# Optimization experiments

Measured on AMD Instinct MI355X. Metric: run time of the kernel, lower is better.

The kernel has to match this reference:

```python
import jax, jax.numpy as jnp
import numpy as np

# Quantization constants from the original module
X_SCALE, X_ZP = 0.0215, -25
Y_SCALE, Y_ZP = 0.0176, 18


def setup_inputs() -> dict:
    key = jax.random.key(0)
    kx, ky = jax.random.split(key)
    K, N = 8192, 16384
    # int8 stand-ins (enum lacks int8); values fit int8 range
    x = jax.random.randint(kx, (K,), 0, 127, dtype=jnp.int32)
    y = jax.random.randint(ky, (K, N), 0, 127, dtype=jnp.int32)
    return {"x": x, "y": y}


def reference(x, y):
    # dequantize_per_tensor: (q - zero_point) * scale, in fp32
    xf = (x.astype(jnp.float32) - X_ZP) * X_SCALE   # [K]
    yf = (y.astype(jnp.float32) - Y_ZP) * Y_SCALE   # [K, N]
    # vector-matrix matmul -> [N]
    return xf @ yf
```

## Files before the change

### kernel.cpp

```cpp
#include <hip/hip_runtime.h>


constexpr int K = 8192;
constexpr int N = 16384;
constexpr float X_SCALE = 0.0215f;
constexpr int   X_ZP    = -25;
constexpr float Y_SCALE = 0.0176f;
constexpr int   Y_ZP    = 18;

constexpr int BLOCK = 256;
constexpr int VEC   = 4;
constexpr int COLS_PER_BLOCK = BLOCK * VEC;
constexpr int NBLK_N = N / COLS_PER_BLOCK;
constexpr int SPLIT_K = 128;
constexpr int KCHUNK = K / SPLIT_K;
constexpr int N4 = N / 4;

typedef int ivec4 __attribute__((ext_vector_type(4)));

__global__ __launch_bounds__(BLOCK, 8) void qgemv_partial(const int* __restrict__ x,
                                                          const ivec4* __restrict__ y,
                                                          ivec4* __restrict__ ws) {
    __shared__ int xs[KCHUNK];

    const int nb = blockIdx.x % NBLK_N;
    const int kc = blockIdx.x / NBLK_N;
    const int k0 = kc * KCHUNK;

    if (threadIdx.x < KCHUNK)
        xs[threadIdx.x] = x[k0 + threadIdx.x] - X_ZP;
    __syncthreads();

    const int col4 = nb * (COLS_PER_BLOCK / 4) + threadIdx.x;
    const ivec4* yv = y + (size_t)k0 * N4 + col4;

    int acc0 = 0, acc1 = 0, acc2 = 0, acc3 = 0;
    int sx = 0;

#pragma unroll 8
    for (int k = 0; k < KCHUNK; ++k) {
        ivec4 v = __builtin_nontemporal_load(&yv[(size_t)k * N4]);
        int a = xs[k];
        sx   += a;
        acc0 += a * v.x;
        acc1 += a * v.y;
        acc2 += a * v.z;
        acc3 += a * v.w;
    }

    const int corr = Y_ZP * sx;
    ivec4 p;
    p.x = acc0 - corr;
    p.y = acc1 - corr;
    p.z = acc2 - corr;
    p.w = acc3 - corr;
    ws[(size_t)kc * N4 + col4] = p;
}

__global__ __launch_bounds__(BLOCK) void qgemv_reduce(const ivec4* __restrict__ ws,
                                                      float* __restrict__ out) {
    const int t = blockIdx.x * BLOCK + threadIdx.x;
    int sx = 0, sy = 0, sz = 0, sw = 0;
#pragma unroll 8
    for (int kc = 0; kc < SPLIT_K; ++kc) {
        ivec4 v = ws[(size_t)kc * N4 + t];
        sx += v.x; sy += v.y; sz += v.z; sw += v.w;
    }
    const float s = X_SCALE * Y_SCALE;
    float4 o;
    o.x = s * (float)sx;
    o.y = s * (float)sy;
    o.z = s * (float)sz;
    o.w = s * (float)sw;
    ((float4*)out)[t] = o;
}

extern "C" void kernel_launch(void* const* d_in, const int* in_sizes, int n_in,
                              void* d_out, int out_size, void* d_ws, size_t ws_size,
                              hipStream_t stream) {
    const int* x = (const int*)d_in[0];
    const ivec4* y = (const ivec4*)d_in[1];
    float* out = (float*)d_out;
    ivec4* ws = (ivec4*)d_ws;

    qgemv_partial<<<NBLK_N * SPLIT_K, BLOCK, 0, stream>>>(x, y, ws);
    qgemv_reduce<<<N4 / BLOCK, BLOCK, 0, stream>>>(ws, out);
}
```

Before: 677.5 us.

## Give each block a full K-row strip and add two-stage split-K reduction

```diff
diff --git a/kernel.cpp b/kernel.cpp
--- a/kernel.cpp
+++ b/kernel.cpp
@@ -9,70 +9,78 @@
 constexpr int   Y_ZP    = 18;
 
 constexpr int BLOCK = 256;
-constexpr int VEC   = 4;
-constexpr int COLS_PER_BLOCK = BLOCK * VEC;
-constexpr int NBLK_N = N / COLS_PER_BLOCK;
-constexpr int SPLIT_K = 128;
+constexpr int N4 = N / 4;
+constexpr int SPLIT_K = 512;
 constexpr int KCHUNK = K / SPLIT_K;
-constexpr int N4 = N / 4;
+constexpr int SEG = N4 / BLOCK;
+
+constexpr int R1 = 64;
+constexpr int R2 = SPLIT_K / R1;
 
 typedef int ivec4 __attribute__((ext_vector_type(4)));
 
-__global__ __launch_bounds__(BLOCK, 8) void qgemv_partial(const int* __restrict__ x,
+__global__ __launch_bounds__(BLOCK, 2) void qgemv_partial(const int* __restrict__ x,
                                                           const ivec4* __restrict__ y,
                                                           ivec4* __restrict__ ws) {
     __shared__ int xs[KCHUNK];
 
-    const int nb = blockIdx.x % NBLK_N;
-    const int kc = blockIdx.x / NBLK_N;
+    const int kc = blockIdx.x;
     const int k0 = kc * KCHUNK;
 
     if (threadIdx.x < KCHUNK)
         xs[threadIdx.x] = x[k0 + threadIdx.x] - X_ZP;
     __syncthreads();
 
-    const int col4 = nb * (COLS_PER_BLOCK / 4) + threadIdx.x;
-    const ivec4* yv = y + (size_t)k0 * N4 + col4;
+    const ivec4* yv = y + (size_t)k0 * N4;
 
-    int acc0 = 0, acc1 = 0, acc2 = 0, acc3 = 0;
+    ivec4 acc[SEG];
+#pragma unroll
+    for (int i = 0; i < SEG; ++i) acc[i] = (ivec4)0;
     int sx = 0;
 
-#pragma unroll 8
     for (int k = 0; k < KCHUNK; ++k) {
-        ivec4 v = __builtin_nontemporal_load(&yv[(size_t)k * N4]);
-        int a = xs[k];
-        sx   += a;
-        acc0 += a * v.x;
-        acc1 += a * v.y;
-        acc2 += a * v.z;
-        acc3 += a * v.w;
+        const int a = xs[k];
+        sx += a;
+        const ivec4* row = yv + (size_t)k * N4;
+#pragma unroll
+        for (int i = 0; i < SEG; ++i) {
+            ivec4 v = __builtin_nontemporal_load(&row[threadIdx.x + BLOCK * i]);
+            acc[i] += v * a;
+        }
     }
 
     const int corr = Y_ZP * sx;
-    ivec4 p;
-    p.x = acc0 - corr;
-    p.y = acc1 - corr;
-    p.z = acc2 - corr;
-    p.w = acc3 - corr;
-    ws[(size_t)kc * N4 + col4] = p;
+    ivec4* wrow = ws + (size_t)kc * N4;
+#pragma unroll
+    for (int i = 0; i < SEG; ++i)
+        wrow[threadIdx.x + BLOCK * i] = acc[i] - corr;
 }
 
-__global__ __launch_bounds__(BLOCK) void qgemv_reduce(const ivec4* __restrict__ ws,
-                                                      float* __restrict__ out) {
-    const int t = blockIdx.x * BLOCK + threadIdx.x;
-    int sx = 0, sy = 0, sz = 0, sw = 0;
+__global__ __launch_bounds__(BLOCK) void qgemv_reduce1(const ivec4* __restrict__ ws,
+                                                       ivec4* __restrict__ ws2) {
+    const int col4 = blockIdx.x * BLOCK + threadIdx.x;
+    const int kb = blockIdx.y;
+    ivec4 s = (ivec4)0;
 #pragma unroll 8
-    for (int kc = 0; kc < SPLIT_K; ++kc) {
-        ivec4 v = ws[(size_t)kc * N4 + t];
-        sx += v.x; sy += v.y; sz += v.z; sw += v.w;
-    }
-    const float s = X_SCALE * Y_SCALE;
+    for (int j = 0; j < R1; ++j)
+        s += ws[(size_t)(kb * R1 + j) * N4 + col4];
+    ws2[(size_t)kb * N4 + col4] = s;
+}
+
+__global__ __launch_bounds__(BLOCK) void qgemv_reduce2(const ivec4* __restrict__ ws2,
+                                                       float* __restrict__ out) {
+    const int col4 = blockIdx.x * BLOCK + threadIdx.x;
+    ivec4 s = (ivec4)0;
+#pragma unroll
+    for (int j = 0; j < R2; ++j)
+        s += ws2[(size_t)j * N4 + col4];
+    const float sc = X_SCALE * Y_SCALE;
     float4 o;
-    o.x = s * (float)sx;
-    o.y = s * (float)sy;
-    o.z = s * (float)sz;
-    o.w = s * (float)sw;
-    ((float4*)out)[t] = o;
+    o.x = sc * (float)s.x;
+    o.y = sc * (float)s.y;
+    o.z = sc * (float)s.z;
+    o.w = sc * (float)s.w;
+    ((float4*)out)[col4] = o;
 }
 
 extern "C" void kernel_launch(void* const* d_in, const int* in_sizes, int n_in,
@@ -81,8 +89,11 @@
     const int* x = (const int*)d_in[0];
     const ivec4* y = (const ivec4*)d_in[1];
     float* out = (float*)d_out;
-    ivec4* ws = (ivec4*)d_ws;
 
-    qgemv_partial<<<NBLK_N * SPLIT_K, BLOCK, 0, stream>>>(x, y, ws);
-    qgemv_reduce<<<N4 / BLOCK, BLOCK, 0, stream>>>(ws, out);
+    ivec4* ws  = (ivec4*)d_ws;
+    ivec4* ws2 = ws + (size_t)SPLIT_K * N4;
+
+    qgemv_partial<<<SPLIT_K, BLOCK, 0, stream>>>(x, y, ws);
+    qgemv_reduce1<<<dim3(N4 / BLOCK, R2), BLOCK, 0, stream>>>(ws, ws2);
+    qgemv_reduce2<<<N4 / BLOCK, BLOCK, 0, stream>>>(ws2, out);
 }
```

Result: no change. 669.6 us (-1.2%).
